# Kernel tuning notes

Measured on AMD Instinct MI355X. Metric: run time of the kernel, lower is better.

## Reference

```python
import jax, jax.numpy as jnp
import numpy as np

N_NODES = 100000


def gcn_conv(x, edge_index, W, b):
    # PyG GCNConv: add self-loops, symmetric normalization D^-1/2 (A+I) D^-1/2
    src, dst = edge_index[0], edge_index[1]
    n = x.shape[0]
    ones = jnp.ones(src.shape[0], dtype=x.dtype)
    deg = jax.ops.segment_sum(ones, dst, num_segments=n) + 1.0  # +1 self-loop
    dinv = jax.lax.rsqrt(deg)
    h = x @ W  # transform first (smaller gather traffic when out_dim < in_dim)
    norm = dinv[src] * dinv[dst]  # [E]
    msg = h[src] * norm[:, None]  # [E, out]
    agg = jax.ops.segment_sum(msg, dst, num_segments=n)
    agg = agg + h * (dinv * dinv)[:, None]  # self-loop contribution
    return agg + b


def setup_inputs() -> dict:
    key = jax.random.key(0)
    k = jax.random.split(key, 8)
    feature_size = 128
    n_edges = 3200000
    x = jax.random.normal(k[0], (N_NODES, feature_size), dtype=jnp.float32)
    edge_index = jax.random.randint(k[1], (2, n_edges), 0, N_NODES, dtype=jnp.int64)
    # Glorot-ish params
    W1 = jax.random.normal(k[2], (feature_size, 64), dtype=jnp.float32) / np.sqrt(feature_size)
    b1 = jnp.zeros((64,), dtype=jnp.float32)
    W2 = jax.random.normal(k[3], (64, 128), dtype=jnp.float32) / np.sqrt(64)
    b2 = jnp.zeros((128,), dtype=jnp.float32)
    Wfc = jax.random.normal(k[4], (128, 1), dtype=jnp.float32) / np.sqrt(128)
    bfc = jnp.zeros((1,), dtype=jnp.float32)
    return {"x": x, "edge_index": edge_index, "W1": W1, "b1": b1,
            "W2": W2, "b2": b2, "Wfc": Wfc, "bfc": bfc}


def reference(x, edge_index, W1, b1, W2, b2, Wfc, bfc):
    h = jax.nn.relu(gcn_conv(x, edge_index, W1, b1))
    h = jax.nn.relu(gcn_conv(h, edge_index, W2, b2))
    return h @ Wfc + bfc  # [N, 1]
```

## Files before the change

### kernel.cpp

```cpp
#include <hip/hip_runtime.h>
#include <hip/hip_fp16.h>

#define NN 100000
#define NBIN 256
#define RANGE 391
#define CAP 16384
#define CAPL 16384

__global__ __launch_bounds__(256) void k_binA(const int* __restrict__ ei_lo,
                                              int E, int* __restrict__ g_bincnt,
                                              unsigned* __restrict__ binbuf) {
    constexpr int ITER = 16;
    __shared__ int cnt[NBIN], basep[NBIN], pos[NBIN];
    __shared__ int s_is64;
    const int t = threadIdx.x;
    const int base = blockIdx.x * (256 * ITER);

    cnt[t] = 0; pos[t] = 0;
    if (t == 0) {
        const unsigned* u = (const unsigned*)ei_lo;
        int is64 = 1;
        for (int i = 0; i < 64; ++i)
            if (u[2 * i + 1] != 0u) { is64 = 0; break; }
        s_is64 = is64;
    }
    __syncthreads();
    const int s = s_is64 ? 2 : 1;

    unsigned pk[ITER];
    int bn[ITER];
#pragma unroll
    for (int i = 0; i < ITER; ++i) {
        int e = base + i * 256 + t;
        if (e < E) {
            int src = __builtin_nontemporal_load(&ei_lo[(long long)s * e]);
            int dst = __builtin_nontemporal_load(&ei_lo[(long long)s * (E + e)]);
            int b = dst / RANGE;
            bn[i] = b;
            pk[i] = ((unsigned)(dst - b * RANGE) << 17) | (unsigned)src;
            atomicAdd(&cnt[b], 1);
        } else bn[i] = -1;
    }
    __syncthreads();
    basep[t] = atomicAdd(&g_bincnt[t], cnt[t]);
    __syncthreads();
#pragma unroll
    for (int i = 0; i < ITER; ++i) {
        if (bn[i] >= 0) {
            int r = atomicAdd(&pos[bn[i]], 1);
            binbuf[(long long)bn[i] * CAP + basep[bn[i]] + r] = pk[i];
        }
    }
}

__global__ __launch_bounds__(512) void k_build(const unsigned* __restrict__ binbuf,
                                               const int* __restrict__ g_bincnt,
                                               int* __restrict__ row_ptr,
                                               float* __restrict__ dinv,
                                               int* __restrict__ csr, int n, int E) {
    __shared__ unsigned ebuf[CAPL];
    __shared__ int cnt[512];
    __shared__ int ssum[256];
    __shared__ int pref[NBIN];
    const int t = threadIdx.x;
    const int bin = blockIdx.x;
    const int lo = bin * RANGE;
    const int rn = min(RANGE, n - lo);
    const int nE = min(g_bincnt[bin], CAPL);
    const unsigned* __restrict__ src = binbuf + (long long)bin * CAP;

    cnt[t] = 0;
    if (t < NBIN) pref[t] = g_bincnt[t];
    __syncthreads();

    for (int i = t; i < nE; i += 512) {
        unsigned e = src[i];
        ebuf[i] = e;
        atomicAdd(&cnt[(int)(e >> 17)], 1);
    }
    __syncthreads();

    for (int off = 1; off < NBIN; off <<= 1) {
        int add = (t >= off && t < NBIN) ? pref[t - off] : 0;
        __syncthreads();
        if (t < NBIN) pref[t] += add;
        __syncthreads();
    }
    const int bstart = (bin > 0) ? pref[bin - 1] : 0;

    int a = 0, b = 0;
    if (t < 256) { a = cnt[2 * t]; b = cnt[2 * t + 1]; ssum[t] = a + b; }
    __syncthreads();
    for (int off = 1; off < 256; off <<= 1) {
        int add = (t >= off && t < 256) ? ssum[t - off] : 0;
        __syncthreads();
        if (t < 256) ssum[t] += add;
        __syncthreads();
    }
    if (t < 256) {
        int prev = (t > 0) ? ssum[t - 1] : 0;
        cnt[2 * t] = prev;
        cnt[2 * t + 1] = prev + a;
        if (2 * t < rn) {
            row_ptr[lo + 2 * t] = bstart + prev;
            dinv[lo + 2 * t] = rsqrtf((float)a + 1.f);
        }
        if (2 * t + 1 < rn) {
            row_ptr[lo + 2 * t + 1] = bstart + prev + a;
            dinv[lo + 2 * t + 1] = rsqrtf((float)b + 1.f);
        }
    }
    if (bin == NBIN - 1 && t == 0) row_ptr[n] = E;
    __syncthreads();

    for (int i = t; i < nE; i += 512) {
        unsigned e = ebuf[i];
        int slot = bstart + atomicAdd(&cnt[(int)(e >> 17)], 1);
        csr[slot] = (int)(e & 0x1FFFFu);
    }
}

__global__ __launch_bounds__(256) void k_gemm1(const float* __restrict__ X,
                                               const float* __restrict__ W,
                                               const float* __restrict__ dinv,
                                               __half* __restrict__ H, int n) {
    constexpr int K = 128, C = 64, RPT = 2;
    constexpr int CG = C / 4, RS = 256 / CG, RT = RS * RPT, XS = K + 4;
    __shared__ float Ws[K * C];
    __shared__ float Xs[RT * XS];
    const int t = threadIdx.x;

    for (int i = t * 4; i < K * C; i += 1024)
        *(float4*)&Ws[i] = *(const float4*)&W[i];

    const int row0 = blockIdx.x * RT;
    for (int i = t * 4; i < RT * K; i += 1024) {
        int r = i / K, k = i % K;
        int gr = row0 + r;
        float4 v = make_float4(0.f, 0.f, 0.f, 0.f);
        if (gr < n) v = *(const float4*)&X[(long long)gr * K + k];
        *(float4*)&Xs[r * XS + k] = v;
    }
    __syncthreads();

    const int cg = t % CG, rs = t / CG;
    float acc[RPT][4];
#pragma unroll
    for (int i = 0; i < RPT; ++i)
#pragma unroll
        for (int j = 0; j < 4; ++j) acc[i][j] = 0.f;

#pragma unroll 2
    for (int k4 = 0; k4 < K / 4; ++k4) {
        float4 xv[RPT];
#pragma unroll
        for (int i = 0; i < RPT; ++i)
            xv[i] = *(float4*)&Xs[(rs * RPT + i) * XS + k4 * 4];
#pragma unroll
        for (int j = 0; j < 4; ++j) {
            float4 w = *(float4*)&Ws[(k4 * 4 + j) * C + cg * 4];
#pragma unroll
            for (int i = 0; i < RPT; ++i) {
                float xvj = (&xv[i].x)[j];
                acc[i][0] = fmaf(xvj, w.x, acc[i][0]);
                acc[i][1] = fmaf(xvj, w.y, acc[i][1]);
                acc[i][2] = fmaf(xvj, w.z, acc[i][2]);
                acc[i][3] = fmaf(xvj, w.w, acc[i][3]);
            }
        }
    }
#pragma unroll
    for (int i = 0; i < RPT; ++i) {
        int gr = row0 + rs * RPT + i;
        if (gr < n) {
            float sc = dinv[gr];
            union { __half h[4]; uint2 u; } pk;
            pk.h[0] = __float2half(acc[i][0] * sc);
            pk.h[1] = __float2half(acc[i][1] * sc);
            pk.h[2] = __float2half(acc[i][2] * sc);
            pk.h[3] = __float2half(acc[i][3] * sc);
            *(uint2*)&H[(long long)gr * C + cg * 4] = pk.u;
        }
    }
}

template <bool RELU>
__global__ __launch_bounds__(256) void k_gather(const __half* __restrict__ h,
                                                const int* __restrict__ row_ptr,
                                                const int* __restrict__ csr,
                                                const float* __restrict__ dinv,
                                                const float* __restrict__ bias,
                                                __half* __restrict__ out, int n) {
    const int node = blockIdx.x * 4 + (threadIdx.x >> 6);
    if (node >= n) return;
    const int lane = threadIdx.x & 63;
    const int g = lane >> 3;
    const int fl = lane & 7;
    const float d = dinv[node];
    const int beg = row_ptr[node], end = row_ptr[node + 1];

    uint4 su = make_uint4(0u, 0u, 0u, 0u);
    if (g == 0) su = *(const uint4*)&h[(long long)node * 64 + fl * 8];

    __half2 z = __float2half2_rn(0.f);
    __half2 acc0 = z, acc1 = z, acc2 = z, acc3 = z;

    const int nfull = (end - beg) >> 4;
    int i = beg;
    for (int it = 0; it < nfull; ++it, i += 16) {
        int s0 = csr[i + g];
        int s1 = csr[i + 8 + g];
        uint4 u0 = *(const uint4*)&h[(long long)s0 * 64 + fl * 8];
        uint4 u1 = *(const uint4*)&h[(long long)s1 * 64 + fl * 8];
        __half2 p0 = __hadd2(*(__half2*)&u0.x, *(__half2*)&u1.x);
        __half2 p1 = __hadd2(*(__half2*)&u0.y, *(__half2*)&u1.y);
        __half2 p2 = __hadd2(*(__half2*)&u0.z, *(__half2*)&u1.z);
        __half2 p3 = __hadd2(*(__half2*)&u0.w, *(__half2*)&u1.w);
        acc0 = __hadd2(acc0, p0);
        acc1 = __hadd2(acc1, p1);
        acc2 = __hadd2(acc2, p2);
        acc3 = __hadd2(acc3, p3);
    }
    if (i + g < end) {
        int s0 = csr[i + g];
        uint4 u0 = *(const uint4*)&h[(long long)s0 * 64 + fl * 8];
        acc0 = __hadd2(acc0, *(__half2*)&u0.x);
        acc1 = __hadd2(acc1, *(__half2*)&u0.y);
        acc2 = __hadd2(acc2, *(__half2*)&u0.z);
        acc3 = __hadd2(acc3, *(__half2*)&u0.w);
    }
    if (i + 8 + g < end) {
        int s1 = csr[i + 8 + g];
        uint4 u1 = *(const uint4*)&h[(long long)s1 * 64 + fl * 8];
        acc0 = __hadd2(acc0, *(__half2*)&u1.x);
        acc1 = __hadd2(acc1, *(__half2*)&u1.y);
        acc2 = __hadd2(acc2, *(__half2*)&u1.z);
        acc3 = __hadd2(acc3, *(__half2*)&u1.w);
    }

    float2 f0 = __half22float2(acc0);
    float2 f1 = __half22float2(acc1);
    float2 f2 = __half22float2(acc2);
    float2 f3 = __half22float2(acc3);
    float r0 = f0.x, r1 = f0.y, r2 = f1.x, r3 = f1.y;
    float r4 = f2.x, r5 = f2.y, r6 = f3.x, r7 = f3.y;
#pragma unroll
    for (int off = 8; off <= 32; off <<= 1) {
        r0 += __shfl_xor(r0, off, 64);
        r1 += __shfl_xor(r1, off, 64);
        r2 += __shfl_xor(r2, off, 64);
        r3 += __shfl_xor(r3, off, 64);
        r4 += __shfl_xor(r4, off, 64);
        r5 += __shfl_xor(r5, off, 64);
        r6 += __shfl_xor(r6, off, 64);
        r7 += __shfl_xor(r7, off, 64);
    }
    if (g == 0) {
        float2 s0 = __half22float2(*(__half2*)&su.x);
        float2 s1 = __half22float2(*(__half2*)&su.y);
        float2 s2 = __half22float2(*(__half2*)&su.z);
        float2 s3 = __half22float2(*(__half2*)&su.w);
        r0 += s0.x; r1 += s0.y; r2 += s1.x; r3 += s1.y;
        r4 += s2.x; r5 += s2.y; r6 += s3.x; r7 += s3.y;
        union { __half hh[8]; uint4 u; } o;
        if (RELU) {
            float4 bv0 = *(const float4*)&bias[fl * 8];
            float4 bv1 = *(const float4*)&bias[fl * 8 + 4];
            o.hh[0] = __float2half(fmaxf(fmaf(d, r0, bv0.x), 0.f) * d);
            o.hh[1] = __float2half(fmaxf(fmaf(d, r1, bv0.y), 0.f) * d);
            o.hh[2] = __float2half(fmaxf(fmaf(d, r2, bv0.z), 0.f) * d);
            o.hh[3] = __float2half(fmaxf(fmaf(d, r3, bv0.w), 0.f) * d);
            o.hh[4] = __float2half(fmaxf(fmaf(d, r4, bv1.x), 0.f) * d);
            o.hh[5] = __float2half(fmaxf(fmaf(d, r5, bv1.y), 0.f) * d);
            o.hh[6] = __float2half(fmaxf(fmaf(d, r6, bv1.z), 0.f) * d);
            o.hh[7] = __float2half(fmaxf(fmaf(d, r7, bv1.w), 0.f) * d);
        } else {
            o.hh[0] = __float2half(d * r0);
            o.hh[1] = __float2half(d * r1);
            o.hh[2] = __float2half(d * r2);
            o.hh[3] = __float2half(d * r3);
            o.hh[4] = __float2half(d * r4);
            o.hh[5] = __float2half(d * r5);
            o.hh[6] = __float2half(d * r6);
            o.hh[7] = __float2half(d * r7);
        }
        *(uint4*)&out[(long long)node * 64 + fl * 8] = o.u;
    }
}

__global__ __launch_bounds__(256) void k_gemm2fc(const __half* __restrict__ G,
                                                 const float* __restrict__ W2,
                                                 const float* __restrict__ b2,
                                                 const float* __restrict__ Wfc,
                                                 const float* __restrict__ bfc,
                                                 float* __restrict__ out, int n) {
    constexpr int K = 64, C = 128, CG = 32, RPT = 4, RT = 32, XS = K + 4;
    __shared__ float Ws[K * C];
    __shared__ float Xs[RT * XS];
    const int t = threadIdx.x;

    for (int i = t * 4; i < K * C; i += 1024)
        *(float4*)&Ws[i] = *(const float4*)&W2[i];

    const int row0 = blockIdx.x * RT;
    for (int i = t * 4; i < RT * K; i += 1024) {
        int r = i / K, k = i % K;
        int gr = row0 + r;
        float4 v = make_float4(0.f, 0.f, 0.f, 0.f);
        if (gr < n) {
            uint2 u = *(const uint2*)&G[(long long)gr * K + k];
            float2 f0 = __half22float2(*(__half2*)&u.x);
            float2 f1 = __half22float2(*(__half2*)&u.y);
            v = make_float4(f0.x, f0.y, f1.x, f1.y);
        }
        *(float4*)&Xs[r * XS + k] = v;
    }
    __syncthreads();

    const int cg = t % CG, rs = t / CG;
    float acc[RPT][4];
#pragma unroll
    for (int i = 0; i < RPT; ++i)
#pragma unroll
        for (int j = 0; j < 4; ++j) acc[i][j] = 0.f;

#pragma unroll 2
    for (int k4 = 0; k4 < K / 4; ++k4) {
        float4 xv[RPT];
#pragma unroll
        for (int i = 0; i < RPT; ++i)
            xv[i] = *(float4*)&Xs[(rs * RPT + i) * XS + k4 * 4];
#pragma unroll
        for (int j = 0; j < 4; ++j) {
            float4 w = *(float4*)&Ws[(k4 * 4 + j) * C + cg * 4];
#pragma unroll
            for (int i = 0; i < RPT; ++i) {
                float xvj = (&xv[i].x)[j];
                acc[i][0] = fmaf(xvj, w.x, acc[i][0]);
                acc[i][1] = fmaf(xvj, w.y, acc[i][1]);
                acc[i][2] = fmaf(xvj, w.z, acc[i][2]);
                acc[i][3] = fmaf(xvj, w.w, acc[i][3]);
            }
        }
    }

    float4 bv = *(const float4*)&b2[cg * 4];
    float4 wf = *(const float4*)&Wfc[cg * 4];
#pragma unroll
    for (int i = 0; i < RPT; ++i) {
        float p = fmaxf(acc[i][0] + bv.x, 0.f) * wf.x
                + fmaxf(acc[i][1] + bv.y, 0.f) * wf.y
                + fmaxf(acc[i][2] + bv.z, 0.f) * wf.z
                + fmaxf(acc[i][3] + bv.w, 0.f) * wf.w;
#pragma unroll
        for (int off = 16; off; off >>= 1) p += __shfl_down(p, off, 32);
        int gr = row0 + rs * RPT + i;
        if (cg == 0 && gr < n) out[gr] = p + bfc[0];
    }
}

extern "C" void kernel_launch(void* const* d_in, const int* in_sizes, int n_in,
                              void* d_out, int out_size, void* d_ws, size_t ws_size,
                              hipStream_t stream) {
    const float* x   = (const float*)d_in[0];
    const void*  ei  = d_in[1];
    const float* W1  = (const float*)d_in[2];
    const float* b1  = (const float*)d_in[3];
    const float* W2  = (const float*)d_in[4];
    const float* b2  = (const float*)d_in[5];
    const float* Wfc = (const float*)d_in[6];
    const float* bfc = (const float*)d_in[7];
    float* out = (float*)d_out;

    const int N = NN;
    const int E = in_sizes[1] / 2;

    char* ws = (char*)d_ws;
    size_t o = 0;
    auto carve = [&](size_t bytes) {
        char* p = ws + o;
        o = (o + bytes + 255) & ~(size_t)255;
        return p;
    };
    float*    dinv      = (float*)carve((size_t)N * 4);
    int*      row_ptr   = (int*)carve((size_t)(N + 1) * 4);
    int*      g_bincnt  = (int*)carve((size_t)NBIN * 4);
    int*      csr       = (int*)carve((size_t)E * 4);
    unsigned* binbuf    = (unsigned*)carve((size_t)NBIN * CAP * 4);
    __half*   bufA      = (__half*)carve((size_t)N * 64 * 2);
    __half*   bufB      = (__half*)carve((size_t)N * 64 * 2);
    __half*   bufG      = (__half*)carve((size_t)N * 64 * 2);

    const int* ei_lo = (const int*)ei;

    hipMemsetAsync(g_bincnt, 0, (size_t)NBIN * 4, stream);
    k_binA<<<(E + 4095) / 4096, 256, 0, stream>>>(ei_lo, E, g_bincnt, binbuf);
    k_build<<<NBIN, 512, 0, stream>>>(binbuf, g_bincnt, row_ptr, dinv, csr, N, E);

    k_gemm1<<<(N + 31) / 32, 256, 0, stream>>>(x, W1, dinv, bufA, N);
    k_gather<true><<<(N + 3) / 4, 256, 0, stream>>>(bufA, row_ptr, csr, dinv, b1, bufB, N);

    k_gather<false><<<(N + 3) / 4, 256, 0, stream>>>(bufB, row_ptr, csr, dinv, nullptr, bufG, N);
    k_gemm2fc<<<(N + 31) / 32, 256, 0, stream>>>(bufG, W2, b2, Wfc, bfc, out, N);
}
```

Baseline: 240.0 us.

## Co-schedule first GEMM tiles with edge binning and CSR build kernels

The X@W1 GEMM is split into tiles that run as extra blocks inside the binning kernel and the CSR-build kernel, so the dense work overlaps the atomic-heavy graph preprocessing. This removes the dependence of GEMM1 on dinv. The dinv row scaling moves into a separate elementwise k_scale pass that re-reads and rewrites the fp16 H buffer. Blocks grow to 512 threads with larger shared memory, which may reduce occupancy. The extra pass adds memory traffic and one more launch.

```diff
diff --git a/kernel.cpp b/kernel.cpp
--- a/kernel.cpp
+++ b/kernel.cpp
@@ -7,134 +7,19 @@
 #define CAP 16384
 #define CAPL 16384
 
-__global__ __launch_bounds__(256) void k_binA(const int* __restrict__ ei_lo,
-                                              int E, int* __restrict__ g_bincnt,
-                                              unsigned* __restrict__ binbuf) {
-    constexpr int ITER = 16;
-    __shared__ int cnt[NBIN], basep[NBIN], pos[NBIN];
-    __shared__ int s_is64;
-    const int t = threadIdx.x;
-    const int base = blockIdx.x * (256 * ITER);
-
-    cnt[t] = 0; pos[t] = 0;
-    if (t == 0) {
-        const unsigned* u = (const unsigned*)ei_lo;
-        int is64 = 1;
-        for (int i = 0; i < 64; ++i)
-            if (u[2 * i + 1] != 0u) { is64 = 0; break; }
-        s_is64 = is64;
-    }
-    __syncthreads();
-    const int s = s_is64 ? 2 : 1;
-
-    unsigned pk[ITER];
-    int bn[ITER];
-#pragma unroll
-    for (int i = 0; i < ITER; ++i) {
-        int e = base + i * 256 + t;
-        if (e < E) {
-            int src = __builtin_nontemporal_load(&ei_lo[(long long)s * e]);
-            int dst = __builtin_nontemporal_load(&ei_lo[(long long)s * (E + e)]);
-            int b = dst / RANGE;
-            bn[i] = b;
-            pk[i] = ((unsigned)(dst - b * RANGE) << 17) | (unsigned)src;
-            atomicAdd(&cnt[b], 1);
-        } else bn[i] = -1;
-    }
-    __syncthreads();
-    basep[t] = atomicAdd(&g_bincnt[t], cnt[t]);
-    __syncthreads();
-#pragma unroll
-    for (int i = 0; i < ITER; ++i) {
-        if (bn[i] >= 0) {
-            int r = atomicAdd(&pos[bn[i]], 1);
-            binbuf[(long long)bn[i] * CAP + basep[bn[i]] + r] = pk[i];
-        }
-    }
-}
-
-__global__ __launch_bounds__(512) void k_build(const unsigned* __restrict__ binbuf,
-                                               const int* __restrict__ g_bincnt,
-                                               int* __restrict__ row_ptr,
-                                               float* __restrict__ dinv,
-                                               int* __restrict__ csr, int n, int E) {
-    __shared__ unsigned ebuf[CAPL];
-    __shared__ int cnt[512];
-    __shared__ int ssum[256];
-    __shared__ int pref[NBIN];
-    const int t = threadIdx.x;
-    const int bin = blockIdx.x;
-    const int lo = bin * RANGE;
-    const int rn = min(RANGE, n - lo);
-    const int nE = min(g_bincnt[bin], CAPL);
-    const unsigned* __restrict__ src = binbuf + (long long)bin * CAP;
-
-    cnt[t] = 0;
-    if (t < NBIN) pref[t] = g_bincnt[t];
-    __syncthreads();
-
-    for (int i = t; i < nE; i += 512) {
-        unsigned e = src[i];
-        ebuf[i] = e;
-        atomicAdd(&cnt[(int)(e >> 17)], 1);
-    }
-    __syncthreads();
-
-    for (int off = 1; off < NBIN; off <<= 1) {
-        int add = (t >= off && t < NBIN) ? pref[t - off] : 0;
-        __syncthreads();
-        if (t < NBIN) pref[t] += add;
-        __syncthreads();
-    }
-    const int bstart = (bin > 0) ? pref[bin - 1] : 0;
-
-    int a = 0, b = 0;
-    if (t < 256) { a = cnt[2 * t]; b = cnt[2 * t + 1]; ssum[t] = a + b; }
-    __syncthreads();
-    for (int off = 1; off < 256; off <<= 1) {
-        int add = (t >= off && t < 256) ? ssum[t - off] : 0;
-        __syncthreads();
-        if (t < 256) ssum[t] += add;
-        __syncthreads();
-    }
-    if (t < 256) {
-        int prev = (t > 0) ? ssum[t - 1] : 0;
-        cnt[2 * t] = prev;
-        cnt[2 * t + 1] = prev + a;
-        if (2 * t < rn) {
-            row_ptr[lo + 2 * t] = bstart + prev;
-            dinv[lo + 2 * t] = rsqrtf((float)a + 1.f);
-        }
-        if (2 * t + 1 < rn) {
-            row_ptr[lo + 2 * t + 1] = bstart + prev + a;
-            dinv[lo + 2 * t + 1] = rsqrtf((float)b + 1.f);
-        }
-    }
-    if (bin == NBIN - 1 && t == 0) row_ptr[n] = E;
-    __syncthreads();
-
-    for (int i = t; i < nE; i += 512) {
-        unsigned e = ebuf[i];
-        int slot = bstart + atomicAdd(&cnt[(int)(e >> 17)], 1);
-        csr[slot] = (int)(e & 0x1FFFFu);
-    }
-}
-
-__global__ __launch_bounds__(256) void k_gemm1(const float* __restrict__ X,
-                                               const float* __restrict__ W,
-                                               const float* __restrict__ dinv,
-                                               __half* __restrict__ H, int n) {
-    constexpr int K = 128, C = 64, RPT = 2;
-    constexpr int CG = C / 4, RS = 256 / CG, RT = RS * RPT, XS = K + 4;
-    __shared__ float Ws[K * C];
-    __shared__ float Xs[RT * XS];
-    const int t = threadIdx.x;
-
-    for (int i = t * 4; i < K * C; i += 1024)
+__device__ __forceinline__ void gemm1_tile(char* smem, int tile,
+                                           const float* __restrict__ X,
+                                           const float* __restrict__ W,
+                                           __half* __restrict__ H, int n, int t) {
+    constexpr int K = 128, C = 64, RPT = 2, CG = 16, RT = 64, XS = K + 4;
+    float* Ws = (float*)smem;
+    float* Xs = (float*)(smem + 32768);
+
+    for (int i = t * 4; i < K * C; i += 2048)
         *(float4*)&Ws[i] = *(const float4*)&W[i];
 
-    const int row0 = blockIdx.x * RT;
-    for (int i = t * 4; i < RT * K; i += 1024) {
+    const int row0 = tile * RT;
+    for (int i = t * 4; i < RT * K; i += 2048) {
         int r = i / K, k = i % K;
         int gr = row0 + r;
         float4 v = make_float4(0.f, 0.f, 0.f, 0.f);
@@ -173,15 +58,158 @@
     for (int i = 0; i < RPT; ++i) {
         int gr = row0 + rs * RPT + i;
         if (gr < n) {
-            float sc = dinv[gr];
             union { __half h[4]; uint2 u; } pk;
-            pk.h[0] = __float2half(acc[i][0] * sc);
-            pk.h[1] = __float2half(acc[i][1] * sc);
-            pk.h[2] = __float2half(acc[i][2] * sc);
-            pk.h[3] = __float2half(acc[i][3] * sc);
+            pk.h[0] = __float2half(acc[i][0]);
+            pk.h[1] = __float2half(acc[i][1]);
+            pk.h[2] = __float2half(acc[i][2]);
+            pk.h[3] = __float2half(acc[i][3]);
             *(uint2*)&H[(long long)gr * C + cg * 4] = pk.u;
         }
     }
+}
+
+__global__ __launch_bounds__(512) void k_binA_gemm1(
+        const int* __restrict__ ei_lo, int E,
+        int* __restrict__ g_bincnt, unsigned* __restrict__ binbuf,
+        const float* __restrict__ X, const float* __restrict__ W1,
+        __half* __restrict__ H, int n, int nBA) {
+    __shared__ alignas(16) char smem[66560];
+    const int t = threadIdx.x;
+    const int b = blockIdx.x;
+    const bool isBin = ((b & 1) == 0) && ((b >> 1) < nBA);
+    if (isBin) {
+        const int blk = b >> 1;
+        int* cnt   = (int*)smem;
+        int* basep = (int*)(smem + 1024);
+        int* pos   = (int*)(smem + 2048);
+        int* pis64 = (int*)(smem + 3072);
+        if (t < NBIN) { cnt[t] = 0; pos[t] = 0; }
+        if (t == 0) {
+            const unsigned* u = (const unsigned*)ei_lo;
+            int is64 = 1;
+            for (int i = 0; i < 64; ++i)
+                if (u[2 * i + 1] != 0u) { is64 = 0; break; }
+            *pis64 = is64;
+        }
+        __syncthreads();
+        const int s = (*pis64) ? 2 : 1;
+        constexpr int ITER = 8;
+        const int base = blk * (512 * ITER);
+        unsigned pk[ITER];
+        int bn[ITER];
+#pragma unroll
+        for (int i = 0; i < ITER; ++i) {
+            int e = base + i * 512 + t;
+            if (e < E) {
+                int src = __builtin_nontemporal_load(&ei_lo[(long long)s * e]);
+                int dst = __builtin_nontemporal_load(&ei_lo[(long long)s * (E + e)]);
+                int bb = dst / RANGE;
+                bn[i] = bb;
+                pk[i] = ((unsigned)(dst - bb * RANGE) << 17) | (unsigned)src;
+                atomicAdd(&cnt[bb], 1);
+            } else bn[i] = -1;
+        }
+        __syncthreads();
+        if (t < NBIN) basep[t] = atomicAdd(&g_bincnt[t], cnt[t]);
+        __syncthreads();
+#pragma unroll
+        for (int i = 0; i < ITER; ++i) {
+            if (bn[i] >= 0) {
+                int r = atomicAdd(&pos[bn[i]], 1);
+                binbuf[(long long)bn[i] * CAP + basep[bn[i]] + r] = pk[i];
+            }
+        }
+    } else {
+        gemm1_tile(smem, b >> 1, X, W1, H, n, t);
+    }
+}
+
+__global__ __launch_bounds__(512) void k_build_gemm1(
+        const unsigned* __restrict__ binbuf, const int* __restrict__ g_bincnt,
+        int* __restrict__ row_ptr, float* __restrict__ dinv, int* __restrict__ csr,
+        int n, int E,
+        const float* __restrict__ X, const float* __restrict__ W1,
+        __half* __restrict__ H, int tile0) {
+    __shared__ alignas(16) char smem[69632];
+    const int t = threadIdx.x;
+    if ((int)blockIdx.x < NBIN) {
+        unsigned* ebuf = (unsigned*)smem;
+        int* cnt  = (int*)(smem + 65536);
+        int* ssum = (int*)(smem + 67584);
+        int* pref = (int*)(smem + 68608);
+        const int bin = blockIdx.x;
+        const int lo = bin * RANGE;
+        const int rn = min(RANGE, n - lo);
+        const int nE = min(g_bincnt[bin], CAPL);
+        const unsigned* __restrict__ src = binbuf + (long long)bin * CAP;
+
+        cnt[t] = 0;
+        if (t < NBIN) pref[t] = g_bincnt[t];
+        __syncthreads();
+
+        for (int i = t; i < nE; i += 512) {
+            unsigned e = src[i];
+            ebuf[i] = e;
+            atomicAdd(&cnt[(int)(e >> 17)], 1);
+        }
+        __syncthreads();
+
+        for (int off = 1; off < NBIN; off <<= 1) {
+            int add = (t >= off && t < NBIN) ? pref[t - off] : 0;
+            __syncthreads();
+            if (t < NBIN) pref[t] += add;
+            __syncthreads();
+        }
+        const int bstart = (bin > 0) ? pref[bin - 1] : 0;
+
+        int a = 0, bcnt = 0;
+        if (t < 256) { a = cnt[2 * t]; bcnt = cnt[2 * t + 1]; ssum[t] = a + bcnt; }
+        __syncthreads();
+        for (int off = 1; off < 256; off <<= 1) {
+            int add = (t >= off && t < 256) ? ssum[t - off] : 0;
+            __syncthreads();
+            if (t < 256) ssum[t] += add;
+            __syncthreads();
+        }
+        if (t < 256) {
+            int prev = (t > 0) ? ssum[t - 1] : 0;
+            cnt[2 * t] = prev;
+            cnt[2 * t + 1] = prev + a;
+            if (2 * t < rn) {
+                row_ptr[lo + 2 * t] = bstart + prev;
+                dinv[lo + 2 * t] = rsqrtf((float)a + 1.f);
+            }
+            if (2 * t + 1 < rn) {
+                row_ptr[lo + 2 * t + 1] = bstart + prev + a;
+                dinv[lo + 2 * t + 1] = rsqrtf((float)bcnt + 1.f);
+            }
+        }
+        if (bin == NBIN - 1 && t == 0) row_ptr[n] = E;
+        __syncthreads();
+
+        for (int i = t; i < nE; i += 512) {
+            unsigned e = ebuf[i];
+            int slot = bstart + atomicAdd(&cnt[(int)(e >> 17)], 1);
+            csr[slot] = (int)(e & 0x1FFFFu);
+        }
+    } else {
+        gemm1_tile(smem, tile0 + ((int)blockIdx.x - NBIN), X, W1, H, n, t);
+    }
+}
+
+__global__ __launch_bounds__(256) void k_scale(__half* __restrict__ h,
+                                               const float* __restrict__ dinv, int n8) {
+    int idx = blockIdx.x * 256 + threadIdx.x;
+    if (idx >= n8) return;
+    float d = dinv[idx >> 3];
+    uint4 u = *(uint4*)&h[(long long)idx * 8];
+    union { __half hh[8]; uint4 u; } o;
+    float2 f;
+    f = __half22float2(*(__half2*)&u.x); o.hh[0] = __float2half(f.x * d); o.hh[1] = __float2half(f.y * d);
+    f = __half22float2(*(__half2*)&u.y); o.hh[2] = __float2half(f.x * d); o.hh[3] = __float2half(f.y * d);
+    f = __half22float2(*(__half2*)&u.z); o.hh[4] = __float2half(f.x * d); o.hh[5] = __float2half(f.y * d);
+    f = __half22float2(*(__half2*)&u.w); o.hh[6] = __float2half(f.x * d); o.hh[7] = __float2half(f.y * d);
+    *(uint4*)&h[(long long)idx * 8] = o.u;
 }
 
 template <bool RELU>
@@ -393,13 +421,19 @@
 
     const int* ei_lo = (const int*)ei;
 
+    const int BA    = (E + 4095) / 4096;
+    const int TILES = (N + 63) / 64;
+    const int T1    = (BA - 1 < TILES) ? (BA - 1) : TILES;
+
     hipMemsetAsync(g_bincnt, 0, (size_t)NBIN * 4, stream);
-    k_binA<<<(E + 4095) / 4096, 256, 0, stream>>>(ei_lo, E, g_bincnt, binbuf);
-    k_build<<<NBIN, 512, 0, stream>>>(binbuf, g_bincnt, row_ptr, dinv, csr, N, E);
-
-    k_gemm1<<<(N + 31) / 32, 256, 0, stream>>>(x, W1, dinv, bufA, N);
+    k_binA_gemm1<<<BA + T1, 512, 0, stream>>>(ei_lo, E, g_bincnt, binbuf,
+                                              x, W1, bufA, N, BA);
+    k_build_gemm1<<<NBIN + (TILES - T1), 512, 0, stream>>>(binbuf, g_bincnt,
+                                                           row_ptr, dinv, csr, N, E,
+                                                           x, W1, bufA, T1);
+    k_scale<<<(N * 8 + 255) / 256, 256, 0, stream>>>(bufA, dinv, N * 8);
+
     k_gather<true><<<(N + 3) / 4, 256, 0, stream>>>(bufA, row_ptr, csr, dinv, b1, bufB, N);
-
     k_gather<false><<<(N + 3) / 4, 256, 0, stream>>>(bufB, row_ptr, csr, dinv, nullptr, bufG, N);
     k_gemm2fc<<<(N + 31) / 32, 256, 0, stream>>>(bufG, W2, b2, Wfc, bfc, out, N);
 }
```

New measurement: 237.2 us. About the same (-1.2%).
